# Performance work log

Measured on AMD Instinct MI355X. Metric: run time of the kernel, lower is better.

Reference implementation:

```python
import jax, jax.numpy as jnp
import numpy as np

B, S = 2, 1024
HIDDEN = 2048
NUM_K, NUM_V = 16, 32
DK, DV = 128, 128
KCONV = 4
EPS = 1e-6
KEY_DIM = NUM_K * DK      # 2048
VAL_DIM = NUM_V * DV      # 4096
RATIO = NUM_V // NUM_K    # 2


def setup_inputs() -> dict:
    key = jax.random.key(0)
    ks = jax.random.split(key, 8)
    sc = lambda k, shape, s=0.02: jax.random.normal(k, shape, jnp.float32) * s
    return {
        "hidden_states": jax.random.normal(ks[0], (B, S, HIDDEN), jnp.float32),
        "W_qkvz": sc(ks[1], (HIDDEN, 2 * KEY_DIM + 2 * VAL_DIM)),
        "W_ba": sc(ks[2], (HIDDEN, 2 * NUM_V)),
        "conv_weight": sc(ks[3], (2 * KEY_DIM + VAL_DIM, KCONV), 0.1),
        "A_log": jnp.log(jax.random.uniform(ks[4], (NUM_V,), jnp.float32, 0.001, 16.0)),
        "dt_bias": jnp.ones((NUM_V,), jnp.float32),
        "norm_weight": jnp.ones((DV,), jnp.float32),
        "W_out": sc(ks[5], (VAL_DIM, HIDDEN)),
    }


def _l2norm(x):
    return x * jax.lax.rsqrt(jnp.sum(x * x, axis=-1, keepdims=True) + 1e-6)


def reference(hidden_states, W_qkvz, W_ba, conv_weight, A_log, dt_bias, norm_weight, W_out):
    Bb, Ss, _ = hidden_states.shape
    # fused in_proj + fix_query_key_value_ordering: per k-head layout [q|k|ratio*v|ratio*z]
    qkvz = (hidden_states @ W_qkvz).reshape(Bb, Ss, NUM_K, 2 * DK + 2 * RATIO * DV)
    q = qkvz[..., :DK]                                        # [B,S,NUM_K,DK]
    k = qkvz[..., DK:2 * DK]
    v = qkvz[..., 2 * DK:2 * DK + RATIO * DV].reshape(Bb, Ss, NUM_V, DV)
    z = qkvz[..., 2 * DK + RATIO * DV:].reshape(Bb, Ss, NUM_V, DV)
    ba = (hidden_states @ W_ba).reshape(Bb, Ss, NUM_K, 2 * RATIO)
    b = ba[..., :RATIO].reshape(Bb, Ss, NUM_V)
    a = ba[..., RATIO:].reshape(Bb, Ss, NUM_V)
    # causal depthwise conv over mixed qkv channels + silu (causal_conv1d)
    mixed = jnp.concatenate(
        [q.reshape(Bb, Ss, -1), k.reshape(Bb, Ss, -1), v.reshape(Bb, Ss, -1)], axis=-1)
    x = jnp.transpose(mixed, (0, 2, 1))                       # [B,C,S]
    x = jnp.pad(x, ((0, 0), (0, 0), (KCONV - 1, 0)))
    conv = jax.lax.conv_general_dilated(
        x, conv_weight[:, None, :], (1,), 'VALID',
        feature_group_count=x.shape[1],
        dimension_numbers=('NCH', 'OIH', 'NCH'))
    mixed = jax.nn.silu(jnp.transpose(conv, (0, 2, 1)))       # [B,S,conv_dim]
    q = mixed[..., :KEY_DIM].reshape(Bb, Ss, NUM_K, DK)
    k = mixed[..., KEY_DIM:2 * KEY_DIM].reshape(Bb, Ss, NUM_K, DK)
    v = mixed[..., 2 * KEY_DIM:].reshape(Bb, Ss, NUM_V, DV)
    # GQA: repeat each k-head to its RATIO consecutive v-heads
    q = jnp.repeat(q, RATIO, axis=2)
    k = jnp.repeat(k, RATIO, axis=2)
    q = _l2norm(q) * (DK ** -0.5)
    k = _l2norm(k)
    # fused_gdn_gating: g = -exp(A_log) * softplus(a + dt_bias); beta = sigmoid(b)
    g = -jnp.exp(A_log) * jax.nn.softplus(a + dt_bias)        # [B,S,H] fp32
    beta = jax.nn.sigmoid(b)
    # recurrent gated delta rule scan; state [B,H,DK,DV]
    def step(state, inp):
        qt, kt, vt, gt, bt = inp
        state = state * jnp.exp(gt)[..., None, None]
        pred = jnp.einsum('bhk,bhkv->bhv', kt, state)
        delta = (vt - pred) * bt[..., None]
        state = state + kt[..., None] * delta[..., None, :]
        out = jnp.einsum('bhk,bhkv->bhv', qt, state)
        return state, out

    xs = (q.transpose(1, 0, 2, 3), k.transpose(1, 0, 2, 3), v.transpose(1, 0, 2, 3),
          g.transpose(1, 0, 2), beta.transpose(1, 0, 2))
    state0 = jnp.zeros((Bb, NUM_V, DK, DV), jnp.float32)
    _, core = jax.lax.scan(step, state0, xs)                  # [S,B,H,DV]
    core = core.transpose(1, 0, 2, 3)
    # RMSNormGated (norm_before_gate=True): rmsnorm(x) * w * silu(z)
    var = jnp.mean(core * core, axis=-1, keepdims=True)
    core = core * jax.lax.rsqrt(var + EPS) * norm_weight * jax.nn.silu(z)
    return core.reshape(Bb, Ss, VAL_DIM) @ W_out              # [B,S,HIDDEN]
```

## Files before the change

kernel.cpp:

```cpp
#include <hip/hip_runtime.h>
#include <stdint.h>

#define B_ 2
#define S_ 1024
#define HID 2048
#define NK 16
#define NV 32
#define DK_ 128
#define DV_ 128
#define QKVZ_N 12288
#define TOK (B_*S_)

typedef unsigned short u16;
typedef __bf16 bf16x8 __attribute__((ext_vector_type(8)));
typedef float f32x4 __attribute__((ext_vector_type(4)));
typedef unsigned short u16x8 __attribute__((ext_vector_type(8)));
typedef unsigned short u16x4 __attribute__((ext_vector_type(4)));

__device__ __forceinline__ float bf2f(u16 u) {
    return __builtin_bit_cast(float, (unsigned)u << 16);
}
__device__ __forceinline__ u16 f2bf(float f) {
    unsigned u = __builtin_bit_cast(unsigned, f);
    u += 0x7fff + ((u >> 16) & 1);
    return (u16)(u >> 16);
}

__device__ __forceinline__ void gl16(const void* g, void* l) {
    __builtin_amdgcn_global_load_lds((const __attribute__((address_space(1))) uint32_t*)g,
                                     (__attribute__((address_space(3))) uint32_t*)l, 16, 0, 0);
}

__device__ __forceinline__ bf16x8 fragld(const u16* base, int row, int col, int rowhw) {
    int idx = row * rowhw + ((((col >> 3) ^ (row & 7))) << 3);
    return __builtin_bit_cast(bf16x8, *(const u16x8*)(base + idx));
}
__device__ __forceinline__ int swzidx(int row, int col, int rowhw) {
    return row * rowhw + (((col >> 3) ^ (row & 7)) << 3) + (col & 7);
}

__global__ void k_cvt_bf16(const float* __restrict__ in, u16* __restrict__ out, int n) {
    int i = (blockIdx.x * blockDim.x + threadIdx.x) * 4;
    if (i >= n) return;
    float4 v = *(const float4*)(in + i);
    u16x4 o = { f2bf(v.x), f2bf(v.y), f2bf(v.z), f2bf(v.w) };
    *(u16x4*)(out + i) = o;
}

__global__ void k_transpose(const float* __restrict__ in, u16* __restrict__ out, int R, int C) {
    __shared__ float tile[32][33];
    int c0 = blockIdx.x * 32, r0 = blockIdx.y * 32;
    int tx = threadIdx.x, ty = threadIdx.y;
#pragma unroll
    for (int i = 0; i < 4; i++)
        tile[ty + i * 8][tx] = in[(size_t)(r0 + ty + i * 8) * C + c0 + tx];
    __syncthreads();
#pragma unroll
    for (int i = 0; i < 4; i++)
        out[(size_t)(c0 + ty + i * 8) * R + r0 + tx] = f2bf(tile[tx][ty + i * 8]);
}

__global__ __launch_bounds__(512) void k_gemm256(const u16* __restrict__ A, const u16* __restrict__ Bt,
                                                 u16* __restrict__ C, int K, int ldc) {
    __shared__ u16 lds[3 * 12288];
    int tid = threadIdx.x, wid = tid >> 6, lane = tid & 63;
    int wm = wid >> 1, wn = wid & 1;
    int l15 = lane & 15, lg = lane >> 4;
    int L = blockIdx.x;
    int xcd = L & 7, j = L >> 3;
    int bn = xcd * 12 + (j >> 3);
    int bm = j & 7;
    const u16* Ag = A + (size_t)bm * 256 * K;
    const u16* Bg = Bt + (size_t)bn * 128 * K;

    auto stage = [&](int t, int b) {
        u16* basebuf = &lds[b * 12288];
        int kcol = t * 32;
#pragma unroll
        for (int jj = 0; jj < 2; jj++) {
            int chunk = wid * 2 + jj;
            int row = chunk * 16 + (lane >> 2);
            int gg = ((lane & 3) + 4 - ((row >> 1) & 3)) & 3;
            gl16(Ag + (size_t)row * K + kcol + gg * 8, (char*)basebuf + chunk * 1024);
        }
        {
            int chunk = wid;
            int row = chunk * 16 + (lane >> 2);
            int gg = ((lane & 3) + 4 - ((row >> 1) & 3)) & 3;
            gl16(Bg + (size_t)row * K + kcol + gg * 8, (char*)(basebuf + 8192) + chunk * 1024);
        }
    };
    auto ldfA = [&](int bsel, int row) -> bf16x8 {
        const u16* p = &lds[bsel * 12288];
        int g = (lg + (row >> 1)) & 3;
        return __builtin_bit_cast(bf16x8, *(const u16x8*)(p + row * 32 + g * 8));
    };
    auto ldfB = [&](int bsel, int row) -> bf16x8 {
        const u16* p = &lds[bsel * 12288 + 8192];
        int g = (lg + (row >> 1)) & 3;
        return __builtin_bit_cast(bf16x8, *(const u16x8*)(p + row * 32 + g * 8));
    };

    f32x4 acc[4][4] = {};
    int NT = K >> 5;
    stage(0, 0);
    stage(1, 1);
    for (int t = 0; t < NT; ++t) {
        if (t < NT - 1) asm volatile("s_waitcnt vmcnt(3) lgkmcnt(0)" ::: "memory");
        else            asm volatile("s_waitcnt vmcnt(0) lgkmcnt(0)" ::: "memory");
        __builtin_amdgcn_s_barrier();
        __builtin_amdgcn_sched_barrier(0);
        if (t + 2 < NT) stage(t + 2, (t + 2) % 3);
        int bsel = t % 3;
        bf16x8 bfr[4];
#pragma unroll
        for (int ni = 0; ni < 4; ni++) bfr[ni] = ldfB(bsel, wn * 64 + ni * 16 + l15);
        __builtin_amdgcn_s_setprio(1);
#pragma unroll
        for (int mi = 0; mi < 4; mi++) {
            bf16x8 af = ldfA(bsel, wm * 64 + mi * 16 + l15);
#pragma unroll
            for (int ni = 0; ni < 4; ni++)
                acc[mi][ni] = __builtin_amdgcn_mfma_f32_16x16x32_bf16(af, bfr[ni], acc[mi][ni], 0, 0, 0);
        }
        __builtin_amdgcn_s_setprio(0);
    }
#pragma unroll
    for (int mi = 0; mi < 4; mi++) {
        int gr0 = bm * 256 + wm * 64 + mi * 16 + lg * 4;
#pragma unroll
        for (int ni = 0; ni < 4; ni++) {
            int gc = bn * 128 + wn * 64 + ni * 16 + l15;
#pragma unroll
            for (int r = 0; r < 4; r++)
                C[(size_t)(gr0 + r) * ldc + gc] = f2bf(acc[mi][ni][r]);
        }
    }
}

template <int OUT_BF16>
__global__ __launch_bounds__(256) void k_gemm(const u16* __restrict__ A, const u16* __restrict__ Bt,
                                              void* __restrict__ Cv, int K, int ldc) {
    __shared__ u16 As[128 * 32];
    __shared__ u16 Bs[128 * 32];
    int tid = threadIdx.x;
    int bm = blockIdx.y, bn = blockIdx.x;
    int wid = tid >> 6, lane = tid & 63;
    int wm = wid >> 1, wn = wid & 1;
    int l15 = lane & 15, lg = lane >> 4;
    const u16* src0 = (wid >> 1) ? (Bt + (size_t)bn * 128 * K) : (A + (size_t)bm * 128 * K);
    u16* ldsb = (wid >> 1) ? Bs : As;
    int cbase = (wid & 1) * 4;
    int lrow = lane >> 2, lcol = (lane & 3) * 8;
    f32x4 acc[4][4] = {};
    for (int k0 = 0; k0 < K; k0 += 32) {
        if (k0) __syncthreads();
#pragma unroll
        for (int c = 0; c < 4; c++) {
            int ch = cbase + c;
            gl16(src0 + (size_t)(16 * ch + lrow) * K + k0 + lcol, (char*)ldsb + ch * 1024);
        }
        __syncthreads();
        bf16x8 af[4], bf[4];
#pragma unroll
        for (int mi = 0; mi < 4; mi++)
            af[mi] = __builtin_bit_cast(bf16x8, *(const u16x8*)&As[(wm * 64 + mi * 16 + l15) * 32 + lg * 8]);
#pragma unroll
        for (int ni = 0; ni < 4; ni++)
            bf[ni] = __builtin_bit_cast(bf16x8, *(const u16x8*)&Bs[(wn * 64 + ni * 16 + l15) * 32 + lg * 8]);
#pragma unroll
        for (int mi = 0; mi < 4; mi++)
#pragma unroll
            for (int ni = 0; ni < 4; ni++)
                acc[mi][ni] = __builtin_amdgcn_mfma_f32_16x16x32_bf16(af[mi], bf[ni], acc[mi][ni], 0, 0, 0);
    }
#pragma unroll
    for (int mi = 0; mi < 4; mi++) {
        int gr0 = bm * 128 + wm * 64 + mi * 16 + lg * 4;
#pragma unroll
        for (int ni = 0; ni < 4; ni++) {
            int gc = bn * 128 + wn * 64 + ni * 16 + l15;
#pragma unroll
            for (int r = 0; r < 4; r++) {
                if (OUT_BF16)
                    ((u16*)Cv)[(size_t)(gr0 + r) * ldc + gc] = f2bf(acc[mi][ni][r]);
                else
                    ((float*)Cv)[(size_t)(gr0 + r) * ldc + gc] = acc[mi][ni][r];
            }
        }
    }
}

__global__ void k_ba(const float* __restrict__ hid, const float* __restrict__ Wba, float* __restrict__ ba) {
    int token = blockIdx.x;
    int c = threadIdx.x;
    const float* h = hid + (size_t)token * HID;
    const float* w = Wba + c;
    float acc = 0.f;
    for (int k = 0; k < HID; k += 4) {
        float4 hv = *(const float4*)(h + k);
        acc += hv.x * w[(size_t)k * 64] + hv.y * w[(size_t)(k + 1) * 64] +
               hv.z * w[(size_t)(k + 2) * 64] + hv.w * w[(size_t)(k + 3) * 64];
    }
    ba[(size_t)token * 64 + c] = acc;
}

__global__ __launch_bounds__(256) void k_conv(const u16* __restrict__ qkvz, const float* __restrict__ ba,
                                              const float* __restrict__ cw, const float* __restrict__ A_log,
                                              const float* __restrict__ dt_bias, u16* __restrict__ qsb,
                                              u16* __restrict__ ksb, u16* __restrict__ vsb,
                                              float2* __restrict__ gb2) {
    __shared__ float sm[4096];
    int token = blockIdx.x;
    int b = token >> 10;
    int t = token & (S_ - 1);
    int tid = threadIdx.x;
    const u16* row3 = qkvz + (size_t)token * QKVZ_N;
#pragma unroll
    for (int i = 0; i < 32; i++) {
        int c = tid + i * 256;
        int col;
        if (c < 2048) col = (c >> 7) * 768 + (c & 127);
        else if (c < 4096) col = ((c - 2048) >> 7) * 768 + 128 + (c & 127);
        else {
            int cc = c - 4096;
            col = (cc >> 8) * 768 + 256 + ((cc >> 7) & 1) * 128 + (cc & 127);
        }
        float4 w = *(const float4*)(cw + c * 4);
        float x3 = bf2f(row3[col]);
        float x2 = (t >= 1) ? bf2f(row3[col - QKVZ_N]) : 0.f;
        float x1 = (t >= 2) ? bf2f(row3[col - 2 * QKVZ_N]) : 0.f;
        float x0 = (t >= 3) ? bf2f(row3[col - 3 * QKVZ_N]) : 0.f;
        float s = w.x * x0 + w.y * x1 + w.z * x2 + w.w * x3;
        s = s / (1.f + __expf(-s));
        if (c < 4096) sm[c] = s;
        else {
            int cc = c - 4096;
            int hv = cc >> 7, d = cc & 127;
            vsb[((size_t)(b * NV + hv) * S_ + t) * 128 + d] = f2bf(s);
        }
    }
    __syncthreads();
    int grp = tid >> 3, l8 = tid & 7;
    float vals[16];
    float ss = 0.f;
    const float* sp = sm + grp * 128 + l8 * 16;
#pragma unroll
    for (int i = 0; i < 16; i++) { vals[i] = sp[i]; ss += vals[i] * vals[i]; }
    ss += __shfl_xor(ss, 1); ss += __shfl_xor(ss, 2); ss += __shfl_xor(ss, 4);
    float scale = rsqrtf(ss + 1e-6f);
    if (grp < 16) scale *= 0.08838834764831845f;
    u16* op = (grp < 16 ? qsb : ksb) + ((size_t)(b * NK + (grp & 15)) * S_ + t) * 128 + l8 * 16;
    u16x8 o0, o1;
#pragma unroll
    for (int i = 0; i < 8; i++) { o0[i] = f2bf(vals[i] * scale); o1[i] = f2bf(vals[i + 8] * scale); }
    *(u16x8*)(op) = o0;
    *(u16x8*)(op + 8) = o1;
    if (tid < 32) {
        int hv = tid;
        float bval = ba[(size_t)token * 64 + (hv >> 1) * 4 + (hv & 1)];
        float aval = ba[(size_t)token * 64 + (hv >> 1) * 4 + 2 + (hv & 1)];
        float x = aval + dt_bias[hv];
        float sp2 = (x > 20.f) ? x : log1pf(__expf(x));
        float graw = -__expf(A_log[hv]) * sp2;
        float bt = 1.f / (1.f + __expf(-bval));
        gb2[(size_t)(b * NV + hv) * S_ + t] = make_float2(graw, bt);
    }
}


__global__ __launch_bounds__(256) void k_prep(const u16* __restrict__ ksb, const u16* __restrict__ qsb,
                                              const float2* __restrict__ gb2, float* __restrict__ Mbuf,
                                              u16* __restrict__ MqB, u16* __restrict__ KtB,
                                              u16* __restrict__ aQB, float* __restrict__ aCB) {
    __shared__ u16 Kl[64 * 128];
    __shared__ u16 Ql[64 * 128];
    __shared__ float QKKK[64 * 68];
    __shared__ float cum[64], bet[64], aex[64], gl[64];
    int bid = blockIdx.x;
    int chunk = bid & 15, hv = (bid >> 4) & 31, b = bid >> 9;
    int hk = hv >> 1;
    size_t ch = bid;
    int tid = threadIdx.x, wid = tid >> 6, lane = tid & 63;
    int l15 = lane & 15, lg = lane >> 4;
    const u16* kg = ksb + ((size_t)(b * NK + hk) * S_ + chunk * 64) * 128;
    const u16* qg = qsb + ((size_t)(b * NK + hk) * S_ + chunk * 64) * 128;
    for (int c = wid; c < 32; c += 4) {
        const u16* src = (c < 16) ? kg : qg;
        u16* dst = (c < 16) ? Kl : Ql;
        int c1 = c & 15;
        int row = c1 * 4 + (lane >> 4);
        int g = lane & 15;
        gl16(src + row * 128 + ((g ^ (row & 7)) << 3), (char*)dst + c1 * 1024 + lane * 16);
    }
    if (tid < 64) {
        float2 gv = gb2[(size_t)(b * NV + hv) * S_ + chunk * 64 + tid];
        gl[tid] = gv.x; bet[tid] = gv.y;
    }
    __syncthreads();
    if (tid == 0) { float s = 0.f; for (int i = 0; i < 64; i++) { s += gl[i]; cum[i] = s; } }
    __syncthreads();
    if (tid < 64) aex[tid] = __expf(cum[tid]);
    {
        f32x4 qk[4] = {};
#pragma unroll
        for (int kk = 0; kk < 4; kk++) {
            bf16x8 af = fragld(Ql, wid * 16 + l15, kk * 32 + lg * 8, 128);
#pragma unroll
            for (int nt = 0; nt < 4; nt++) {
                bf16x8 bk = fragld(Kl, nt * 16 + l15, kk * 32 + lg * 8, 128);
                qk[nt] = __builtin_amdgcn_mfma_f32_16x16x32_bf16(af, bk, qk[nt], 0, 0, 0);
            }
        }
#pragma unroll
        for (int nt = 0; nt < 4; nt++)
#pragma unroll
            for (int r = 0; r < 4; r++)
                QKKK[(wid * 16 + lg * 4 + r) * 68 + nt * 16 + l15] = qk[nt][r];
    }
    __syncthreads();
    {
        int i = tid >> 2, jc = (tid & 3) * 16;
        u16x8 m0, m1;
#pragma unroll
        for (int jj = 0; jj < 16; jj++) {
            int j = jc + jj;
            float v = (j <= i) ? __expf(cum[i] - cum[j]) * QKKK[i * 68 + j] : 0.f;
            if (jj < 8) m0[jj] = f2bf(v); else m1[jj - 8] = f2bf(v);
        }
        *(u16x8*)(MqB + ch * 4096 + i * 64 + jc) = m0;
        *(u16x8*)(MqB + ch * 4096 + i * 64 + jc + 8) = m1;
    }
    __syncthreads();
    {
        f32x4 kkc[4] = {};
#pragma unroll
        for (int kk = 0; kk < 4; kk++) {
            bf16x8 af = fragld(Kl, wid * 16 + l15, kk * 32 + lg * 8, 128);
#pragma unroll
            for (int nt = 0; nt < 4; nt++) {
                bf16x8 bk = fragld(Kl, nt * 16 + l15, kk * 32 + lg * 8, 128);
                kkc[nt] = __builtin_amdgcn_mfma_f32_16x16x32_bf16(af, bk, kkc[nt], 0, 0, 0);
            }
        }
        __syncthreads();
#pragma unroll
        for (int nt = 0; nt < 4; nt++)
#pragma unroll
            for (int r = 0; r < 4; r++)
                QKKK[(wid * 16 + lg * 4 + r) * 68 + nt * 16 + l15] = kkc[nt][r];
    }
    __syncthreads();
    {
        int i = tid >> 2, jc = (tid & 3) * 16;
        float4 out4;
#pragma unroll
        for (int q4 = 0; q4 < 4; q4++) {
#pragma unroll
            for (int e = 0; e < 4; e++) {
                int j = jc + q4 * 4 + e;
                float v = (j < i) ? bet[i] * __expf(cum[i] - cum[j]) * QKKK[i * 68 + j] : 0.f;
                ((float*)&out4)[e] = v;
            }
            *(float4*)(Mbuf + ch * 4096 + i * 64 + jc + q4 * 4) = out4;
        }
    }
    {
        int dk = tid >> 1, jc = (tid & 1) * 32;
#pragma unroll
        for (int q8 = 0; q8 < 4; q8++) {
            u16x8 o;
#pragma unroll
            for (int e = 0; e < 8; e++) {
                int j = jc + q8 * 8 + e;
                o[e] = f2bf(__expf(cum[63] - cum[j]) * bf2f(Kl[swzidx(j, dk, 128)]));
            }
            *(u16x8*)(KtB + ch * 8192 + dk * 64 + jc + q8 * 8) = o;
        }
    }
    {
        int i = tid >> 2, dc = (tid & 3) * 32;
        float a = aex[i];
#pragma unroll
        for (int q8 = 0; q8 < 4; q8++) {
            u16x8 o;
#pragma unroll
            for (int e = 0; e < 8; e++)
                o[e] = f2bf(a * bf2f(Ql[swzidx(i, dc + q8 * 8 + e, 128)]));
            *(u16x8*)(aQB + ch * 8192 + i * 128 + dc + q8 * 8) = o;
        }
    }
    if (tid == 0) aCB[ch] = aex[63];
}

__global__ __launch_bounds__(256) void k_solve(const u16* __restrict__ ksb, const u16* __restrict__ vsb,
                                               const float2* __restrict__ gb2, const float* __restrict__ Mbuf,
                                               float* __restrict__ TvB, u16* __restrict__ WB) {
    __shared__ float Ml[64 * 64];
    __shared__ u16 Kl[64 * 128];
    __shared__ u16 Vl[64 * 128];
    __shared__ u16 bounce[64 * 136];
    __shared__ float cum[64], bet[64], aex[64], gl[64];
    int bid = blockIdx.x;
    int chunk = bid & 15, hv = (bid >> 4) & 31, b = bid >> 9;
    int hk = hv >> 1;
    size_t ch = bid;
    int tid = threadIdx.x, wid = tid >> 6, lane = tid & 63;
    const u16* kg = ksb + ((size_t)(b * NK + hk) * S_ + chunk * 64) * 128;
    const u16* vg = vsb + ((size_t)(b * NV + hv) * S_ + chunk * 64) * 128;
    const float* mg = Mbuf + ch * 4096;
    for (int c = wid; c < 48; c += 4) {
        if (c < 16) gl16((const char*)mg + c * 1024 + lane * 16, (char*)Ml + c * 1024 + lane * 16);
        else if (c < 32) gl16((const char*)kg + (c - 16) * 1024 + lane * 16, (char*)Kl + (c - 16) * 1024 + lane * 16);
        else gl16((const char*)vg + (c - 32) * 1024 + lane * 16, (char*)Vl + (c - 32) * 1024 + lane * 16);
    }
    if (tid < 64) {
        float2 gv = gb2[(size_t)(b * NV + hv) * S_ + chunk * 64 + tid];
        gl[tid] = gv.x; bet[tid] = gv.y;
    }
    __syncthreads();
    if (tid == 0) { float s = 0.f; for (int i = 0; i < 64; i++) { s += gl[i]; cum[i] = s; } }
    __syncthreads();
    if (tid < 64) aex[tid] = __expf(cum[tid]);
    __syncthreads();
    int c = tid;
    float X[64];
    if (c < 128) {
#pragma unroll
        for (int i = 0; i < 64; i++) X[i] = bet[i] * bf2f(Vl[i * 128 + c]);
    } else {
        int d = c - 128;
#pragma unroll
        for (int i = 0; i < 64; i++) X[i] = -bet[i] * aex[i] * bf2f(Kl[i * 128 + d]);
    }
#pragma unroll
    for (int IB = 0; IB < 8; ++IB) {
#pragma unroll
        for (int JB = 0; JB < IB; ++JB) {
#pragma unroll
            for (int ii = 0; ii < 8; ++ii) {
                const float* mr = &Ml[(IB * 8 + ii) * 64 + JB * 8];
                float4 a = *(const float4*)mr, bq = *(const float4*)(mr + 4);
                float x = X[IB * 8 + ii];
                x = fmaf(-a.x, X[JB * 8 + 0], x); x = fmaf(-a.y, X[JB * 8 + 1], x);
                x = fmaf(-a.z, X[JB * 8 + 2], x); x = fmaf(-a.w, X[JB * 8 + 3], x);
                x = fmaf(-bq.x, X[JB * 8 + 4], x); x = fmaf(-bq.y, X[JB * 8 + 5], x);
                x = fmaf(-bq.z, X[JB * 8 + 6], x); x = fmaf(-bq.w, X[JB * 8 + 7], x);
                X[IB * 8 + ii] = x;
            }
        }
#pragma unroll
        for (int ii = 1; ii < 8; ++ii) {
            float x = X[IB * 8 + ii];
#pragma unroll
            for (int jj = 0; jj < ii; ++jj)
                x = fmaf(-Ml[(IB * 8 + ii) * 64 + IB * 8 + jj], X[IB * 8 + jj], x);
            X[IB * 8 + ii] = x;
        }
    }
    if (c < 128) {
        float* o = TvB + ch * 8192 + (size_t)c * 64;
#pragma unroll
        for (int q4 = 0; q4 < 16; q4++) {
            float4 v4 = { X[q4 * 4], X[q4 * 4 + 1], X[q4 * 4 + 2], X[q4 * 4 + 3] };
            *(float4*)(o + q4 * 4) = v4;
        }
    } else {
        int d = c - 128;
#pragma unroll
        for (int i = 0; i < 64; i++) bounce[i * 136 + d] = f2bf(X[i]);
    }
    __syncthreads();
    {
        int i = tid >> 2, dc = (tid & 3) * 32;
#pragma unroll
        for (int q8 = 0; q8 < 4; q8++) {
            u16x8 o;
#pragma unroll
            for (int e = 0; e < 8; e++) o[e] = bounce[i * 136 + dc + q8 * 8 + e];
            *(u16x8*)(WB + ch * 8192 + i * 128 + dc + q8 * 8) = o;
        }
    }
}

__global__ __launch_bounds__(256) void k_chunk(const float* __restrict__ TvB, const u16* __restrict__ WB,
                                               const u16* __restrict__ aQB, const u16* __restrict__ MqB,
                                               const u16* __restrict__ KtB, const float* __restrict__ aCB,
                                               float* __restrict__ core) {
    __shared__ u16 S0h[64 * 128], S0l[64 * 128];
    __shared__ u16 DTh[64 * 64], DTl[64 * 64];
    __shared__ float Tvl[64 * 64];
    __shared__ u16 Wl[64 * 128], aQl[64 * 128];
    __shared__ u16 Mql[64 * 64];
    __shared__ u16 Ktl[128 * 64];
    int bid = blockIdx.x;
    int split = bid & 1, bh = bid >> 1;
    int tid = threadIdx.x, wid = tid >> 6, lane = tid & 63;
    int l15 = lane & 15, lg = lane >> 4;
    float4 z4 = {0.f, 0.f, 0.f, 0.f};
    for (int i = tid; i < 64 * 128 / 8; i += 256) {
        *(float4*)(S0h + i * 8) = z4;
        *(float4*)(S0l + i * 8) = z4;
    }
    for (int chunk = 0; chunk < 16; ++chunk) {
        size_t ch = (size_t)bh * 16 + chunk;
        const char* tvg = (const char*)(TvB + ch * 8192 + (size_t)split * 64 * 64);
        const char* wg = (const char*)(WB + ch * 8192);
        const char* qg = (const char*)(aQB + ch * 8192);
        const char* mg = (const char*)(MqB + ch * 4096);
        const char* kg = (const char*)(KtB + ch * 8192);
        for (int c = wid; c < 72; c += 4) {
            if (c < 16) {
                gl16(tvg + c * 1024 + lane * 16, (char*)Tvl + c * 1024 + lane * 16);
            } else if (c < 32) {
                int cc = c - 16; int row = cc * 4 + (lane >> 4); int g = lane & 15;
                gl16(wg + row * 256 + ((g ^ (row & 7)) << 4), (char*)Wl + cc * 1024 + lane * 16);
            } else if (c < 48) {
                int cc = c - 32; int row = cc * 4 + (lane >> 4); int g = lane & 15;
                gl16(qg + row * 256 + ((g ^ (row & 7)) << 4), (char*)aQl + cc * 1024 + lane * 16);
            } else if (c < 56) {
                int cc = c - 48; int row = cc * 8 + (lane >> 3); int g = lane & 7;
                gl16(mg + row * 128 + ((g ^ (row & 7)) << 4), (char*)Mql + cc * 1024 + lane * 16);
            } else {
                int cc = c - 56; int row = cc * 8 + (lane >> 3); int g = lane & 7;
                gl16(kg + row * 128 + ((g ^ (row & 7)) << 4), (char*)Ktl + cc * 1024 + lane * 16);
            }
        }
        float aC = aCB[ch];
        __syncthreads();
        f32x4 Dacc[4], Oacc[4] = {};
#pragma unroll
        for (int nt = 0; nt < 4; nt++)
#pragma unroll
            for (int r = 0; r < 4; r++)
                Dacc[nt][r] = Tvl[(wid * 16 + lg * 4 + r) * 64 + nt * 16 + l15];
#pragma unroll
        for (int kk = 0; kk < 4; kk++) {
            bf16x8 aH = fragld(S0h, wid * 16 + l15, kk * 32 + lg * 8, 128);
            bf16x8 aL = fragld(S0l, wid * 16 + l15, kk * 32 + lg * 8, 128);
#pragma unroll
            for (int nt = 0; nt < 4; nt++) {
                bf16x8 bW = fragld(Wl, nt * 16 + l15, kk * 32 + lg * 8, 128);
                Dacc[nt] = __builtin_amdgcn_mfma_f32_16x16x32_bf16(aH, bW,
                           __builtin_amdgcn_mfma_f32_16x16x32_bf16(aL, bW, Dacc[nt], 0, 0, 0), 0, 0, 0);
                bf16x8 bQ = fragld(aQl, nt * 16 + l15, kk * 32 + lg * 8, 128);
                Oacc[nt] = __builtin_amdgcn_mfma_f32_16x16x32_bf16(aH, bQ,
                           __builtin_amdgcn_mfma_f32_16x16x32_bf16(aL, bQ, Oacc[nt], 0, 0, 0), 0, 0, 0);
            }
        }
#pragma unroll
        for (int nt = 0; nt < 4; nt++)
#pragma unroll
            for (int r = 0; r < 4; r++) {
                int dv = wid * 16 + lg * 4 + r, t = nt * 16 + l15;
                float x = Dacc[nt][r];
                u16 h = f2bf(x);
                int idx = swzidx(dv, t, 64);
                DTh[idx] = h; DTl[idx] = f2bf(x - bf2f(h));
            }
#pragma unroll
        for (int kk2 = 0; kk2 < 2; kk2++) {
            bf16x8 aDh = fragld(DTh, wid * 16 + l15, kk2 * 32 + lg * 8, 64);
            bf16x8 aDl = fragld(DTl, wid * 16 + l15, kk2 * 32 + lg * 8, 64);
#pragma unroll
            for (int nt = 0; nt < 4; nt++) {
                bf16x8 bM = fragld(Mql, nt * 16 + l15, kk2 * 32 + lg * 8, 64);
                Oacc[nt] = __builtin_amdgcn_mfma_f32_16x16x32_bf16(aDh, bM,
                           __builtin_amdgcn_mfma_f32_16x16x32_bf16(aDl, bM, Oacc[nt], 0, 0, 0), 0, 0, 0);
            }
        }
#pragma unroll
        for (int nt = 0; nt < 4; nt++) {
            float4 o = { Oacc[nt][0], Oacc[nt][1], Oacc[nt][2], Oacc[nt][3] };
            size_t t = (size_t)chunk * 64 + nt * 16 + l15;
            *(float4*)(core + ((size_t)bh * S_ + t) * 128 + split * 64 + wid * 16 + lg * 4) = o;
        }
        f32x4 Sacc[8] = {};
#pragma unroll
        for (int kk2 = 0; kk2 < 2; kk2++) {
            bf16x8 aDh = fragld(DTh, wid * 16 + l15, kk2 * 32 + lg * 8, 64);
            bf16x8 aDl = fragld(DTl, wid * 16 + l15, kk2 * 32 + lg * 8, 64);
#pragma unroll
            for (int nd = 0; nd < 8; nd++) {
                bf16x8 bK = fragld(Ktl, nd * 16 + l15, kk2 * 32 + lg * 8, 64);
                Sacc[nd] = __builtin_amdgcn_mfma_f32_16x16x32_bf16(aDh, bK,
                           __builtin_amdgcn_mfma_f32_16x16x32_bf16(aDl, bK, Sacc[nd], 0, 0, 0), 0, 0, 0);
            }
        }
#pragma unroll
        for (int nd = 0; nd < 8; nd++)
#pragma unroll
            for (int r = 0; r < 4; r++) {
                int dv = wid * 16 + lg * 4 + r, dk = nd * 16 + l15;
                int idx = swzidx(dv, dk, 128);
                float old = bf2f(S0h[idx]) + bf2f(S0l[idx]);
                float nu = fmaf(aC, old, Sacc[nd][r]);
                u16 h = f2bf(nu);
                S0h[idx] = h; S0l[idx] = f2bf(nu - bf2f(h));
            }
        __syncthreads();
    }
}

__global__ __launch_bounds__(256) void k_gate(const float* __restrict__ core, const u16* __restrict__ qkvz,
                                              const float* __restrict__ nw, u16* __restrict__ gated) {
    int token = blockIdx.x, tid = threadIdx.x;
    int b = token >> 10, t = token & (S_ - 1);
    int grp = tid >> 3, l8 = tid & 7;
    const float* cp = core + ((size_t)(b * NV + grp) * S_ + t) * DV_ + l8 * 16;
    float vals[16];
    float ss = 0.f;
#pragma unroll
    for (int i = 0; i < 16; i++) { vals[i] = cp[i]; ss += vals[i] * vals[i]; }
    ss += __shfl_xor(ss, 1); ss += __shfl_xor(ss, 2); ss += __shfl_xor(ss, 4);
    float rms = rsqrtf(ss * (1.0f / DV_) + 1e-6f);
    const u16* zp = qkvz + (size_t)token * QKVZ_N + (grp >> 1) * 768 + 512 + (grp & 1) * 128 + l8 * 16;
    u16* op = gated + ((size_t)token * NV + grp) * DV_ + l8 * 16;
#pragma unroll
    for (int i = 0; i < 16; i++) {
        float z = bf2f(zp[i]);
        float sz = z / (1.f + __expf(-z));
        op[i] = f2bf(vals[i] * rms * nw[l8 * 16 + i] * sz);
    }
}

extern "C" void kernel_launch(void* const* d_in, const int* in_sizes, int n_in,
                              void* d_out, int out_size, void* d_ws, size_t ws_size,
                              hipStream_t stream) {
    const float* hidden = (const float*)d_in[0];
    const float* Wqkvz = (const float*)d_in[1];
    const float* Wba = (const float*)d_in[2];
    const float* convw = (const float*)d_in[3];
    const float* A_log = (const float*)d_in[4];
    const float* dt_bias = (const float*)d_in[5];
    const float* norm_w = (const float*)d_in[6];
    const float* Wout = (const float*)d_in[7];

    char* ws = (char*)d_ws;
    size_t off = 0;
    auto alloc = [&](size_t bytes) -> void* {
        void* p = ws + off;
        off += (bytes + 255) & ~(size_t)255;
        return p;
    };
    u16* hiddenB = (u16*)alloc((size_t)TOK * HID * 2);
    u16* WqT = (u16*)alloc((size_t)QKVZ_N * HID * 2);
    u16* WoT = (u16*)alloc((size_t)HID * 4096 * 2);
    u16* qkvz = (u16*)alloc((size_t)TOK * QKVZ_N * 2);
    float* ba = (float*)alloc((size_t)TOK * 64 * 4);
    u16* qsb = (u16*)alloc((size_t)B_ * NK * S_ * 128 * 2);
    u16* ksb = (u16*)alloc((size_t)B_ * NK * S_ * 128 * 2);
    u16* vsb = (u16*)alloc((size_t)B_ * NV * S_ * 128 * 2);
    float2* gb2 = (float2*)alloc((size_t)B_ * NV * S_ * 8);
    float* Mbuf = (float*)alloc((size_t)1024 * 4096 * 4);
    u16* MqB = (u16*)alloc((size_t)1024 * 4096 * 2);
    u16* KtB = (u16*)alloc((size_t)1024 * 8192 * 2);
    u16* aQB = (u16*)alloc((size_t)1024 * 8192 * 2);
    float* TvB = (float*)alloc((size_t)1024 * 8192 * 4);
    u16* WB = (u16*)alloc((size_t)1024 * 8192 * 2);
    float* aCB = (float*)alloc((size_t)1024 * 4);
    float* core = (float*)alloc((size_t)B_ * NV * S_ * 128 * 4);
    u16* gated = (u16*)alloc((size_t)TOK * 4096 * 2);

    k_cvt_bf16<<<4096, 256, 0, stream>>>(hidden, hiddenB, TOK * HID);
    k_transpose<<<dim3(QKVZ_N / 32, HID / 32), dim3(32, 8), 0, stream>>>(Wqkvz, WqT, HID, QKVZ_N);
    k_transpose<<<dim3(HID / 32, 4096 / 32), dim3(32, 8), 0, stream>>>(Wout, WoT, 4096, HID);
    k_gemm256<<<768, 512, 0, stream>>>(hiddenB, WqT, qkvz, HID, QKVZ_N);
    k_ba<<<TOK, 64, 0, stream>>>(hidden, Wba, ba);
    k_conv<<<TOK, 256, 0, stream>>>(qkvz, ba, convw, A_log, dt_bias, qsb, ksb, vsb, gb2);
    k_prep<<<1024, 256, 0, stream>>>(ksb, qsb, gb2, Mbuf, MqB, KtB, aQB, aCB);
    k_solve<<<1024, 256, 0, stream>>>(ksb, vsb, gb2, Mbuf, TvB, WB);
    k_chunk<<<128, 256, 0, stream>>>(TvB, WB, aQB, MqB, KtB, aCB, core);
    k_gate<<<TOK, 256, 0, stream>>>(core, qkvz, norm_w, gated);
    k_gemm<0><<<dim3(HID / 128, TOK / 128), 256, 0, stream>>>(gated, WoT, d_out, 4096, HID);
}
```

Measured before the change: 556.7 us.

## Fuse solve into prep kernel and double-buffer chunk-scan operand loads

Merges k_solve into k_prep so the decay-masked KK matrix stays in shared memory instead of round-tripping through a global Mbuf. The K/Q/V tiles and cumulative gates are loaded once, and the swizzled K layout is now indexed correctly in the solve stage. In k_chunk, W, aQ and Kt tiles are double-buffered so the next chunk's loads are issued while the current chunk computes, and Tv and Mq are read straight from global memory into registers. This trades extra LDS per block (lower occupancy in the fused kernel) and uncached direct global reads for fewer launches, less global traffic and overlapped loads.

```diff
diff --git a/kernel.cpp b/kernel.cpp
--- a/kernel.cpp
+++ b/kernel.cpp
@@ -270,12 +270,16 @@
 
 
 __global__ __launch_bounds__(256) void k_prep(const u16* __restrict__ ksb, const u16* __restrict__ qsb,
-                                              const float2* __restrict__ gb2, float* __restrict__ Mbuf,
+                                              const u16* __restrict__ vsb, const float2* __restrict__ gb2,
                                               u16* __restrict__ MqB, u16* __restrict__ KtB,
-                                              u16* __restrict__ aQB, float* __restrict__ aCB) {
+                                              u16* __restrict__ aQB, float* __restrict__ aCB,
+                                              float* __restrict__ TvB, u16* __restrict__ WB) {
     __shared__ u16 Kl[64 * 128];
     __shared__ u16 Ql[64 * 128];
+    __shared__ u16 Vl[64 * 128];
     __shared__ float QKKK[64 * 68];
+    __shared__ float Ml[64 * 64];
+    __shared__ u16 bounce[64 * 136];
     __shared__ float cum[64], bet[64], aex[64], gl[64];
     int bid = blockIdx.x;
     int chunk = bid & 15, hv = (bid >> 4) & 31, b = bid >> 9;
@@ -285,13 +289,19 @@
     int l15 = lane & 15, lg = lane >> 4;
     const u16* kg = ksb + ((size_t)(b * NK + hk) * S_ + chunk * 64) * 128;
     const u16* qg = qsb + ((size_t)(b * NK + hk) * S_ + chunk * 64) * 128;
-    for (int c = wid; c < 32; c += 4) {
-        const u16* src = (c < 16) ? kg : qg;
-        u16* dst = (c < 16) ? Kl : Ql;
-        int c1 = c & 15;
-        int row = c1 * 4 + (lane >> 4);
-        int g = lane & 15;
-        gl16(src + row * 128 + ((g ^ (row & 7)) << 3), (char*)dst + c1 * 1024 + lane * 16);
+    const u16* vg = vsb + ((size_t)(b * NV + hv) * S_ + chunk * 64) * 128;
+    for (int c = wid; c < 48; c += 4) {
+        if (c < 32) {
+            const u16* src = (c < 16) ? kg : qg;
+            u16* dst = (c < 16) ? Kl : Ql;
+            int c1 = c & 15;
+            int row = c1 * 4 + (lane >> 4);
+            int g = lane & 15;
+            gl16(src + row * 128 + ((g ^ (row & 7)) << 3), (char*)dst + c1 * 1024 + lane * 16);
+        } else {
+            int c1 = c - 32;
+            gl16((const char*)vg + c1 * 1024 + lane * 16, (char*)Vl + c1 * 1024 + lane * 16);
+        }
     }
     if (tid < 64) {
         float2 gv = gb2[(size_t)(b * NV + hv) * S_ + chunk * 64 + tid];
@@ -362,7 +372,7 @@
                 float v = (j < i) ? bet[i] * __expf(cum[i] - cum[j]) * QKKK[i * 68 + j] : 0.f;
                 ((float*)&out4)[e] = v;
             }
-            *(float4*)(Mbuf + ch * 4096 + i * 64 + jc + q4 * 4) = out4;
+            *(float4*)(&Ml[i * 64 + jc + q4 * 4]) = out4;
         }
     }
     {
@@ -391,37 +401,6 @@
         }
     }
     if (tid == 0) aCB[ch] = aex[63];
-}
-
-__global__ __launch_bounds__(256) void k_solve(const u16* __restrict__ ksb, const u16* __restrict__ vsb,
-                                               const float2* __restrict__ gb2, const float* __restrict__ Mbuf,
-                                               float* __restrict__ TvB, u16* __restrict__ WB) {
-    __shared__ float Ml[64 * 64];
-    __shared__ u16 Kl[64 * 128];
-    __shared__ u16 Vl[64 * 128];
-    __shared__ u16 bounce[64 * 136];
-    __shared__ float cum[64], bet[64], aex[64], gl[64];
-    int bid = blockIdx.x;
-    int chunk = bid & 15, hv = (bid >> 4) & 31, b = bid >> 9;
-    int hk = hv >> 1;
-    size_t ch = bid;
-    int tid = threadIdx.x, wid = tid >> 6, lane = tid & 63;
-    const u16* kg = ksb + ((size_t)(b * NK + hk) * S_ + chunk * 64) * 128;
-    const u16* vg = vsb + ((size_t)(b * NV + hv) * S_ + chunk * 64) * 128;
-    const float* mg = Mbuf + ch * 4096;
-    for (int c = wid; c < 48; c += 4) {
-        if (c < 16) gl16((const char*)mg + c * 1024 + lane * 16, (char*)Ml + c * 1024 + lane * 16);
-        else if (c < 32) gl16((const char*)kg + (c - 16) * 1024 + lane * 16, (char*)Kl + (c - 16) * 1024 + lane * 16);
-        else gl16((const char*)vg + (c - 32) * 1024 + lane * 16, (char*)Vl + (c - 32) * 1024 + lane * 16);
-    }
-    if (tid < 64) {
-        float2 gv = gb2[(size_t)(b * NV + hv) * S_ + chunk * 64 + tid];
-        gl[tid] = gv.x; bet[tid] = gv.y;
-    }
-    __syncthreads();
-    if (tid == 0) { float s = 0.f; for (int i = 0; i < 64; i++) { s += gl[i]; cum[i] = s; } }
-    __syncthreads();
-    if (tid < 64) aex[tid] = __expf(cum[tid]);
     __syncthreads();
     int c = tid;
     float X[64];
@@ -431,7 +410,7 @@
     } else {
         int d = c - 128;
 #pragma unroll
-        for (int i = 0; i < 64; i++) X[i] = -bet[i] * aex[i] * bf2f(Kl[i * 128 + d]);
+        for (int i = 0; i < 64; i++) X[i] = -bet[i] * aex[i] * bf2f(Kl[swzidx(i, d, 128)]);
     }
 #pragma unroll
     for (int IB = 0; IB < 8; ++IB) {
@@ -489,10 +468,9 @@
                                                float* __restrict__ core) {
     __shared__ u16 S0h[64 * 128], S0l[64 * 128];
     __shared__ u16 DTh[64 * 64], DTl[64 * 64];
-    __shared__ float Tvl[64 * 64];
-    __shared__ u16 Wl[64 * 128], aQl[64 * 128];
-    __shared__ u16 Mql[64 * 64];
-    __shared__ u16 Ktl[128 * 64];
+    __shared__ u16 Wl[2][64 * 128];
+    __shared__ u16 aQl[2][64 * 128];
+    __shared__ u16 Ktl[2][128 * 64];
     int bid = blockIdx.x;
     int split = bid & 1, bh = bid >> 1;
     int tid = threadIdx.x, wid = tid >> 6, lane = tid & 63;
@@ -502,48 +480,57 @@
         *(float4*)(S0h + i * 8) = z4;
         *(float4*)(S0l + i * 8) = z4;
     }
-    for (int chunk = 0; chunk < 16; ++chunk) {
+    auto stage = [&](int chunk, int bufi) {
         size_t ch = (size_t)bh * 16 + chunk;
-        const char* tvg = (const char*)(TvB + ch * 8192 + (size_t)split * 64 * 64);
         const char* wg = (const char*)(WB + ch * 8192);
         const char* qg = (const char*)(aQB + ch * 8192);
-        const char* mg = (const char*)(MqB + ch * 4096);
         const char* kg = (const char*)(KtB + ch * 8192);
-        for (int c = wid; c < 72; c += 4) {
+        for (int c = wid; c < 48; c += 4) {
             if (c < 16) {
-                gl16(tvg + c * 1024 + lane * 16, (char*)Tvl + c * 1024 + lane * 16);
+                int row = c * 4 + (lane >> 4); int g = lane & 15;
+                gl16(wg + row * 256 + ((g ^ (row & 7)) << 4), (char*)&Wl[bufi][0] + c * 1024 + lane * 16);
             } else if (c < 32) {
                 int cc = c - 16; int row = cc * 4 + (lane >> 4); int g = lane & 15;
-                gl16(wg + row * 256 + ((g ^ (row & 7)) << 4), (char*)Wl + cc * 1024 + lane * 16);
-            } else if (c < 48) {
-                int cc = c - 32; int row = cc * 4 + (lane >> 4); int g = lane & 15;
-                gl16(qg + row * 256 + ((g ^ (row & 7)) << 4), (char*)aQl + cc * 1024 + lane * 16);
-            } else if (c < 56) {
-                int cc = c - 48; int row = cc * 8 + (lane >> 3); int g = lane & 7;
-                gl16(mg + row * 128 + ((g ^ (row & 7)) << 4), (char*)Mql + cc * 1024 + lane * 16);
+                gl16(qg + row * 256 + ((g ^ (row & 7)) << 4), (char*)&aQl[bufi][0] + cc * 1024 + lane * 16);
             } else {
-                int cc = c - 56; int row = cc * 8 + (lane >> 3); int g = lane & 7;
-                gl16(kg + row * 128 + ((g ^ (row & 7)) << 4), (char*)Ktl + cc * 1024 + lane * 16);
-            }
-        }
+                int cc = c - 32; int row = cc * 8 + (lane >> 3); int g = lane & 7;
+                gl16(kg + row * 128 + ((g ^ (row & 7)) << 4), (char*)&Ktl[bufi][0] + cc * 1024 + lane * 16);
+            }
+        }
+    };
+    stage(0, 0);
+    for (int chunk = 0; chunk < 16; ++chunk) {
+        int cur = chunk & 1;
+        size_t ch = (size_t)bh * 16 + chunk;
         float aC = aCB[ch];
-        __syncthreads();
+        asm volatile("s_waitcnt vmcnt(0) lgkmcnt(0)" ::: "memory");
+        __builtin_amdgcn_s_barrier();
+        __builtin_amdgcn_sched_barrier(0);
+        if (chunk < 15) stage(chunk + 1, cur ^ 1);
         f32x4 Dacc[4], Oacc[4] = {};
+        const float* tvg = TvB + ch * 8192 + (size_t)(split * 64) * 64;
 #pragma unroll
         for (int nt = 0; nt < 4; nt++)
 #pragma unroll
             for (int r = 0; r < 4; r++)
-                Dacc[nt][r] = Tvl[(wid * 16 + lg * 4 + r) * 64 + nt * 16 + l15];
+                Dacc[nt][r] = tvg[(size_t)(wid * 16 + lg * 4 + r) * 64 + nt * 16 + l15];
+        bf16x8 bMreg[2][4];
+#pragma unroll
+        for (int kk2 = 0; kk2 < 2; kk2++)
+#pragma unroll
+            for (int nt = 0; nt < 4; nt++)
+                bMreg[kk2][nt] = __builtin_bit_cast(bf16x8,
+                    *(const u16x8*)(MqB + ch * 4096 + (size_t)(nt * 16 + l15) * 64 + kk2 * 32 + lg * 8));
 #pragma unroll
         for (int kk = 0; kk < 4; kk++) {
             bf16x8 aH = fragld(S0h, wid * 16 + l15, kk * 32 + lg * 8, 128);
             bf16x8 aL = fragld(S0l, wid * 16 + l15, kk * 32 + lg * 8, 128);
 #pragma unroll
             for (int nt = 0; nt < 4; nt++) {
-                bf16x8 bW = fragld(Wl, nt * 16 + l15, kk * 32 + lg * 8, 128);
+                bf16x8 bW = fragld(&Wl[cur][0], nt * 16 + l15, kk * 32 + lg * 8, 128);
                 Dacc[nt] = __builtin_amdgcn_mfma_f32_16x16x32_bf16(aH, bW,
                            __builtin_amdgcn_mfma_f32_16x16x32_bf16(aL, bW, Dacc[nt], 0, 0, 0), 0, 0, 0);
-                bf16x8 bQ = fragld(aQl, nt * 16 + l15, kk * 32 + lg * 8, 128);
+                bf16x8 bQ = fragld(&aQl[cur][0], nt * 16 + l15, kk * 32 + lg * 8, 128);
                 Oacc[nt] = __builtin_amdgcn_mfma_f32_16x16x32_bf16(aH, bQ,
                            __builtin_amdgcn_mfma_f32_16x16x32_bf16(aL, bQ, Oacc[nt], 0, 0, 0), 0, 0, 0);
             }
@@ -564,9 +551,8 @@
             bf16x8 aDl = fragld(DTl, wid * 16 + l15, kk2 * 32 + lg * 8, 64);
 #pragma unroll
             for (int nt = 0; nt < 4; nt++) {
-                bf16x8 bM = fragld(Mql, nt * 16 + l15, kk2 * 32 + lg * 8, 64);
-                Oacc[nt] = __builtin_amdgcn_mfma_f32_16x16x32_bf16(aDh, bM,
-                           __builtin_amdgcn_mfma_f32_16x16x32_bf16(aDl, bM, Oacc[nt], 0, 0, 0), 0, 0, 0);
+                Oacc[nt] = __builtin_amdgcn_mfma_f32_16x16x32_bf16(aDh, bMreg[kk2][nt],
+                           __builtin_amdgcn_mfma_f32_16x16x32_bf16(aDl, bMreg[kk2][nt], Oacc[nt], 0, 0, 0), 0, 0, 0);
             }
         }
 #pragma unroll
@@ -582,7 +568,7 @@
             bf16x8 aDl = fragld(DTl, wid * 16 + l15, kk2 * 32 + lg * 8, 64);
 #pragma unroll
             for (int nd = 0; nd < 8; nd++) {
-                bf16x8 bK = fragld(Ktl, nd * 16 + l15, kk2 * 32 + lg * 8, 64);
+                bf16x8 bK = fragld(&Ktl[cur][0], nd * 16 + l15, kk2 * 32 + lg * 8, 64);
                 Sacc[nd] = __builtin_amdgcn_mfma_f32_16x16x32_bf16(aDh, bK,
                            __builtin_amdgcn_mfma_f32_16x16x32_bf16(aDl, bK, Sacc[nd], 0, 0, 0), 0, 0, 0);
             }
@@ -598,7 +584,6 @@
                 u16 h = f2bf(nu);
                 S0h[idx] = h; S0l[idx] = f2bf(nu - bf2f(h));
             }
-        __syncthreads();
     }
 }
 
@@ -652,7 +637,6 @@
     u16* ksb = (u16*)alloc((size_t)B_ * NK * S_ * 128 * 2);
     u16* vsb = (u16*)alloc((size_t)B_ * NV * S_ * 128 * 2);
     float2* gb2 = (float2*)alloc((size_t)B_ * NV * S_ * 8);
-    float* Mbuf = (float*)alloc((size_t)1024 * 4096 * 4);
     u16* MqB = (u16*)alloc((size_t)1024 * 4096 * 2);
     u16* KtB = (u16*)alloc((size_t)1024 * 8192 * 2);
     u16* aQB = (u16*)alloc((size_t)1024 * 8192 * 2);
@@ -668,8 +652,7 @@
     k_gemm256<<<768, 512, 0, stream>>>(hiddenB, WqT, qkvz, HID, QKVZ_N);
     k_ba<<<TOK, 64, 0, stream>>>(hidden, Wba, ba);
     k_conv<<<TOK, 256, 0, stream>>>(qkvz, ba, convw, A_log, dt_bias, qsb, ksb, vsb, gb2);
-    k_prep<<<1024, 256, 0, stream>>>(ksb, qsb, gb2, Mbuf, MqB, KtB, aQB, aCB);
-    k_solve<<<1024, 256, 0, stream>>>(ksb, vsb, gb2, Mbuf, TvB, WB);
+    k_prep<<<1024, 256, 0, stream>>>(ksb, qsb, vsb, gb2, MqB, KtB, aQB, aCB, TvB, WB);
     k_chunk<<<128, 256, 0, stream>>>(TvB, WB, aQB, MqB, KtB, aCB, core);
     k_gate<<<TOK, 256, 0, stream>>>(core, qkvz, norm_w, gated);
     k_gemm<0><<<dim3(HID / 128, TOK / 128), 256, 0, stream>>>(gated, WoT, d_out, 4096, HID);
```

Result: slower. 576.0 us (+3.5%).
